# Performance work log

Hardware: AMD Instinct MI355X
Metric: run time of the kernel (lower is better)

## Reference

```python
import jax, jax.numpy as jnp
import numpy as np

B, T, I, H, L, O = 256, 512, 5, 100, 5, 3
BN_EPS = 1e-5


def _lstm_layer(xs, W_ih, W_hh, bias):
    """xs: [B,T,in] -> hidden seq [B,T,H]. PyTorch gate order i,f,g,o."""
    Bv = xs.shape[0]
    Hd = W_hh.shape[1]
    h0 = jnp.zeros((Bv, Hd), xs.dtype)
    c0 = jnp.zeros((Bv, Hd), xs.dtype)

    def step(carry, x_t):
        h, c = carry
        gates = x_t @ W_ih.T + h @ W_hh.T + bias  # [B,4H]
        i, f, g, o = jnp.split(gates, 4, axis=-1)
        i = jax.nn.sigmoid(i)
        f = jax.nn.sigmoid(f)
        g = jnp.tanh(g)
        o = jax.nn.sigmoid(o)
        c = f * c + i * g
        h = o * jnp.tanh(c)
        return (h, c), h

    _, hs = jax.lax.scan(step, (h0, c0), xs.transpose(1, 0, 2))  # hs: [T,B,H]
    return hs.transpose(1, 0, 2)


def setup_inputs() -> dict:
    key = jax.random.key(0)
    ks = jax.random.split(key, 12)
    s = 0.1  # weight scale to keep gates in a reasonable range
    return {
        "x": jax.random.normal(ks[0], (B, T, I), jnp.float32),
        "W_ih0": jax.random.normal(ks[1], (4 * H, I), jnp.float32) * s,
        "W_hh0": jax.random.normal(ks[2], (4 * H, H), jnp.float32) * s,
        "b0": jax.random.normal(ks[3], (4 * H,), jnp.float32) * s,
        "W_ih": jax.random.normal(ks[4], (L - 1, 4 * H, H), jnp.float32) * s,
        "W_hh": jax.random.normal(ks[5], (L - 1, 4 * H, H), jnp.float32) * s,
        "b": jax.random.normal(ks[6], (L - 1, 4 * H), jnp.float32) * s,
        "gamma": jnp.ones((H,), jnp.float32),
        "beta": jnp.zeros((H,), jnp.float32),
        "run_mean": jnp.zeros((H,), jnp.float32),
        "run_var": jnp.ones((H,), jnp.float32),
        "W1": jax.random.normal(ks[7], (H, H), jnp.float32) * s,
        "b1": jnp.zeros((H,), jnp.float32),
        "W2": jax.random.normal(ks[8], (H, H), jnp.float32) * s,
        "b2": jnp.zeros((H,), jnp.float32),
        "W3": jax.random.normal(ks[9], (O, H), jnp.float32) * s,
        "b3": jnp.zeros((O,), jnp.float32),
    }


def reference(x, W_ih0, W_hh0, b0, W_ih, W_hh, b,
              gamma, beta, run_mean, run_var,
              W1, b1, W2, b2, W3, b3):
    # 5-layer stacked LSTM (batch_first)
    h = _lstm_layer(x, W_ih0, W_hh0, b0)
    for l in range(L - 1):
        h = _lstm_layer(h, W_ih[l], W_hh[l], b[l])
    # dropout (eval mode -> identity), take last timestep
    last = h[:, -1, :]  # [B,H]
    # BatchNorm1d, eval mode (running statistics)
    xn = (last - run_mean) * jax.lax.rsqrt(run_var + BN_EPS) * gamma + beta
    # 3-layer MLP head with ReLU
    y = jax.nn.relu(xn @ W1.T + b1)
    y = jax.nn.relu(y @ W2.T + b2)
    return y @ W3.T + b3  # [B,O]
```

## Files before the change

kernel.cpp:

```cpp
#include <hip/hip_runtime.h>

#define NT 1024
#define TSEQ 512

typedef float float2v __attribute__((ext_vector_type(2)));

__device__ __forceinline__ float sigmoid_(float x) { return 1.0f / (1.0f + __expf(-x)); }
__device__ __forceinline__ float tanh_(float x) { return 1.0f - 2.0f / (1.0f + __expf(2.0f * x)); }

extern "C" __global__ void prep_weights(const float* __restrict__ Wih0,
                                        const float* __restrict__ Whh0,
                                        const float* __restrict__ WihL,
                                        const float* __restrict__ WhhL,
                                        float4* __restrict__ wbuf) {
    int gid = blockIdx.x * 256 + threadIdx.x;
    if (gid >= 102400) return;
    int tid = gid & 1023;
    int lgq = gid >> 10;
    int gq = lgq % 20;
    int l = lgq / 20;
    int g = gq / 5, q = gq % 5;
    float tmp[4] = {0.f, 0.f, 0.f, 0.f};
    if (tid < 1000) {
        int f = tid / 100, rg = tid % 100;
        int row = g * 100 + rg;
        int k0 = 20 * f + 4 * q;
        for (int c = 0; c < 4; ++c) {
            int k = k0 + c;
            float w = 0.f;
            if (l == 0) {
                if (k < 5) w = Wih0[row * 5 + k];
                else if (k < 105) w = Whh0[row * 100 + (k - 5)];
            } else {
                if (k < 100) w = WihL[(l - 1) * 40000 + row * 100 + k];
                else w = WhhL[(l - 1) * 40000 + row * 100 + (k - 100)];
            }
            tmp[c] = w;
        }
    }
    wbuf[gid] = make_float4(tmp[0], tmp[1], tmp[2], tmp[3]);
}

template <int IN, bool FIRST, bool STORE>
__device__ void run_layer(const float4* __restrict__ wl, const float* __restrict__ bL,
                          const float* __restrict__ xsrc, float* __restrict__ hdst,
                          int b, int tid, int f, int rg, bool real,
                          float* xh, float4* part4) {
    float2v w[40];
#pragma unroll
    for (int g = 0; g < 4; ++g) {
#pragma unroll
        for (int q = 0; q < 5; ++q) {
            float4 t = wl[(g * 5 + q) * 1024 + tid];
            w[g * 10 + 2 * q]     = (float2v){t.x, t.y};
            w[g * 10 + 2 * q + 1] = (float2v){t.z, t.w};
        }
    }
    float bi = 0.f, bf = 0.f, bg = 0.f, bo = 0.f;
    if (tid < 100) {
        bi = bL[tid]; bf = bL[100 + tid]; bg = bL[200 + tid]; bo = bL[300 + tid];
    }

    if (tid < 256) xh[tid] = 0.f;
    __syncthreads();
    if (FIRST) {
        if (tid < 5) xh[tid] = xsrc[b * TSEQ * 5 + tid];
    } else {
        if (tid < 25) ((float4*)xh)[tid] = ((const float4*)xsrc)[b * TSEQ * 25 + tid];
    }
    __syncthreads();

    const float4* xv4 = (const float4*)xh + f * 5;
    float c = 0.f, hprev = 0.f;

    for (int t = 0; t < TSEQ; ++t) {
        if (STORE) {
            if (tid < 100 && t > 0) hdst[(b * TSEQ + (t - 1)) * 100 + tid] = hprev;
        }
        int tn = (t + 1 < TSEQ) ? (t + 1) : (TSEQ - 1);
        float pfs = 0.f;
        float4 pf4 = {0.f, 0.f, 0.f, 0.f};
        if (FIRST) {
            if (tid >= 128 && tid < 133) pfs = xsrc[(b * TSEQ + tn) * 5 + (tid - 128)];
        } else {
            if (tid >= 128 && tid < 153) pf4 = ((const float4*)xsrc)[(b * TSEQ + tn) * 25 + (tid - 128)];
        }

        float2v a0 = {0.f, 0.f}, a1 = {0.f, 0.f}, a2 = {0.f, 0.f}, a3 = {0.f, 0.f};
#pragma unroll
        for (int q = 0; q < 5; ++q) {
            float4 xq = xv4[q];
            float2v xlo = (float2v){xq.x, xq.y};
            float2v xhi = (float2v){xq.z, xq.w};
            a0 = __builtin_elementwise_fma(w[2 * q],      xlo, a0);
            a0 = __builtin_elementwise_fma(w[2 * q + 1],  xhi, a0);
            a1 = __builtin_elementwise_fma(w[10 + 2 * q],     xlo, a1);
            a1 = __builtin_elementwise_fma(w[10 + 2 * q + 1], xhi, a1);
            a2 = __builtin_elementwise_fma(w[20 + 2 * q],     xlo, a2);
            a2 = __builtin_elementwise_fma(w[20 + 2 * q + 1], xhi, a2);
            a3 = __builtin_elementwise_fma(w[30 + 2 * q],     xlo, a3);
            a3 = __builtin_elementwise_fma(w[30 + 2 * q + 1], xhi, a3);
        }
        if (real) {
            part4[f * 100 + rg] = make_float4(a0.x + a0.y, a1.x + a1.y,
                                              a2.x + a2.y, a3.x + a3.y);
        }
        __syncthreads();

        if (tid < 100) {
            float4 s = part4[tid];
#pragma unroll
            for (int ff = 1; ff < 10; ++ff) {
                float4 tt = part4[ff * 100 + tid];
                s.x += tt.x; s.y += tt.y; s.z += tt.z; s.w += tt.w;
            }
            float gi = sigmoid_(s.x + bi);
            float gf = sigmoid_(s.y + bf);
            float gg = tanh_(s.z + bg);
            float go = sigmoid_(s.w + bo);
            c = gf * c + gi * gg;
            float hv = go * tanh_(c);
            xh[IN + tid] = hv;
            hprev = hv;
        }
        if (FIRST) {
            if (tid >= 128 && tid < 133) xh[tid - 128] = pfs;
        } else {
            if (tid >= 128 && tid < 153) ((float4*)xh)[tid - 128] = pf4;
        }
        __syncthreads();
    }
    if (STORE) {
        if (tid < 100) hdst[(b * TSEQ + TSEQ - 1) * 100 + tid] = hprev;
    }
}

extern "C" __global__ void __launch_bounds__(NT, 4)
gesture_lstm_kernel(const float* __restrict__ x,
                    const float4* __restrict__ wbuf,
                    const float* __restrict__ b0, const float* __restrict__ bLv,
                    const float* __restrict__ gamma, const float* __restrict__ beta,
                    const float* __restrict__ rmean, const float* __restrict__ rvar,
                    const float* __restrict__ W1, const float* __restrict__ b1,
                    const float* __restrict__ W2, const float* __restrict__ b2,
                    const float* __restrict__ W3, const float* __restrict__ b3,
                    float* __restrict__ out, float* __restrict__ hseq) {
    __shared__ __align__(16) float xh[256];
    __shared__ __align__(16) float4 part4[1000];
    __shared__ __align__(16) float hw[10000];

    int tid = threadIdx.x;
    int b = blockIdx.x;
    int f = tid / 100;
    int rg = tid % 100;
    bool real = tid < 1000;

    run_layer<5,   true,  true >(wbuf + 0 * 20480, b0,         x,    hseq, b, tid, f, rg, real, xh, part4);
    run_layer<100, false, true >(wbuf + 1 * 20480, bLv + 0,    hseq, hseq, b, tid, f, rg, real, xh, part4);
    run_layer<100, false, true >(wbuf + 2 * 20480, bLv + 400,  hseq, hseq, b, tid, f, rg, real, xh, part4);
    run_layer<100, false, true >(wbuf + 3 * 20480, bLv + 800,  hseq, hseq, b, tid, f, rg, real, xh, part4);
    run_layer<100, false, false>(wbuf + 4 * 20480, bLv + 1200, hseq, hseq, b, tid, f, rg, real, xh, part4);

    float* fcbuf = (float*)part4;
    if (tid < 100) {
        float hv = xh[100 + tid];
        xh[tid] = (hv - rmean[tid]) * rsqrtf(rvar[tid] + 1e-5f) * gamma[tid] + beta[tid];
    }
    __syncthreads();

    for (int i = tid; i < 2500; i += NT) ((float4*)hw)[i] = ((const float4*)W1)[i];
    __syncthreads();
    if (tid < 100) {
        float acc = b1[tid];
#pragma unroll
        for (int k = 0; k < 100; ++k) acc = fmaf(hw[tid * 100 + k], xh[k], acc);
        fcbuf[tid] = fmaxf(acc, 0.0f);
    }
    __syncthreads();

    for (int i = tid; i < 2500; i += NT) ((float4*)hw)[i] = ((const float4*)W2)[i];
    __syncthreads();
    if (tid < 100) {
        float acc = b2[tid];
#pragma unroll
        for (int k = 0; k < 100; ++k) acc = fmaf(hw[tid * 100 + k], fcbuf[k], acc);
        fcbuf[400 + tid] = fmaxf(acc, 0.0f);
    }
    __syncthreads();

    if (tid < 3) {
        float acc = b3[tid];
#pragma unroll
        for (int k = 0; k < 100; ++k) acc = fmaf(W3[tid * 100 + k], fcbuf[400 + k], acc);
        out[b * 3 + tid] = acc;
    }
}

extern "C" void kernel_launch(void* const* d_in, const int* in_sizes, int n_in,
                              void* d_out, int out_size, void* d_ws, size_t ws_size,
                              hipStream_t stream) {
    const float* x     = (const float*)d_in[0];
    const float* Wih0  = (const float*)d_in[1];
    const float* Whh0  = (const float*)d_in[2];
    const float* b0    = (const float*)d_in[3];
    const float* WihL  = (const float*)d_in[4];
    const float* WhhL  = (const float*)d_in[5];
    const float* bLv   = (const float*)d_in[6];
    const float* gamma = (const float*)d_in[7];
    const float* beta  = (const float*)d_in[8];
    const float* rmean = (const float*)d_in[9];
    const float* rvar  = (const float*)d_in[10];
    const float* W1    = (const float*)d_in[11];
    const float* b1    = (const float*)d_in[12];
    const float* W2    = (const float*)d_in[13];
    const float* b2    = (const float*)d_in[14];
    const float* W3    = (const float*)d_in[15];
    const float* b3    = (const float*)d_in[16];

    float4* wbuf = (float4*)d_ws;
    float* hseq  = (float*)((char*)d_ws + 102400 * 16);

    prep_weights<<<dim3(400), dim3(256), 0, stream>>>(Wih0, Whh0, WihL, WhhL, wbuf);
    gesture_lstm_kernel<<<dim3(256), dim3(NT), 0, stream>>>(
        x, wbuf, b0, bLv, gamma, beta, rmean, rvar, W1, b1, W2, b2, W3, b3,
        (float*)d_out, hseq);
}
```

Measured before the change: 2.435 ms.

## Replace LDS partial-sum reduction with DPP cross-lane reduction and double-buffered state

Reorganizes the per-step LSTM work so each group of 16 lanes owns two hidden units across all four gates, with the k-dimension split across the 16 lanes. Partial dot products are combined with DPP lane shuffles instead of being written to shared memory and summed by 100 threads. The hidden/input vector is double-buffered, which cuts the two barriers per timestep down to one. The block shrinks to 832 threads and each thread keeps 28 float4 weight registers, raising register pressure. The activation math is now done redundantly by all lanes.

Measured after the change: 9.624 ms. 3.95x slower.

```diff
diff --git a/kernel.cpp b/kernel.cpp
--- a/kernel.cpp
+++ b/kernel.cpp
@@ -1,12 +1,18 @@
 #include <hip/hip_runtime.h>
 
-#define NT 1024
+#define NT 832
 #define TSEQ 512
 
 typedef float float2v __attribute__((ext_vector_type(2)));
 
 __device__ __forceinline__ float sigmoid_(float x) { return 1.0f / (1.0f + __expf(-x)); }
 __device__ __forceinline__ float tanh_(float x) { return 1.0f - 2.0f / (1.0f + __expf(2.0f * x)); }
+
+template <int CTRL>
+__device__ __forceinline__ float dppmv(float x) {
+    return __int_as_float(__builtin_amdgcn_update_dpp(
+        0, __float_as_int(x), CTRL, 0xF, 0xF, true));
+}
 
 extern "C" __global__ void prep_weights(const float* __restrict__ Wih0,
                                         const float* __restrict__ Whh0,
@@ -14,28 +20,30 @@
                                         const float* __restrict__ WhhL,
                                         float4* __restrict__ wbuf) {
     int gid = blockIdx.x * 256 + threadIdx.x;
-    if (gid >= 102400) return;
-    int tid = gid & 1023;
-    int lgq = gid >> 10;
-    int gq = lgq % 20;
-    int l = lgq / 20;
-    int g = gq / 5, q = gq % 5;
+    if (gid >= 116480) return;
+    int tid = gid % 832;
+    int ql = gid / 832;
+    int q = ql % 28;
+    int l = ql / 28;
+    int p = tid / 16, f = tid % 16;
     float tmp[4] = {0.f, 0.f, 0.f, 0.f};
-    if (tid < 1000) {
-        int f = tid / 100, rg = tid % 100;
-        int row = g * 100 + rg;
-        int k0 = 20 * f + 4 * q;
-        for (int c = 0; c < 4; ++c) {
-            int k = k0 + c;
+    if (tid < 800) {
+        for (int j = 0; j < 4; ++j) {
+            int e = 4 * q + j;
+            int r = e / 14, cc = e % 14;
+            int unit = 2 * p + (r >= 4 ? 1 : 0);
+            int gate = r & 3;
+            int row = gate * 100 + unit;
+            int k = 14 * f + cc;
             float w = 0.f;
             if (l == 0) {
                 if (k < 5) w = Wih0[row * 5 + k];
                 else if (k < 105) w = Whh0[row * 100 + (k - 5)];
             } else {
                 if (k < 100) w = WihL[(l - 1) * 40000 + row * 100 + k];
-                else w = WhhL[(l - 1) * 40000 + row * 100 + (k - 100)];
+                else if (k < 200) w = WhhL[(l - 1) * 40000 + row * 100 + (k - 100)];
             }
-            tmp[c] = w;
+            tmp[j] = w;
         }
     }
     wbuf[gid] = make_float4(tmp[0], tmp[1], tmp[2], tmp[3]);
@@ -44,98 +52,102 @@
 template <int IN, bool FIRST, bool STORE>
 __device__ void run_layer(const float4* __restrict__ wl, const float* __restrict__ bL,
                           const float* __restrict__ xsrc, float* __restrict__ hdst,
-                          int b, int tid, int f, int rg, bool real,
-                          float* xh, float4* part4) {
-    float2v w[40];
-#pragma unroll
-    for (int g = 0; g < 4; ++g) {
-#pragma unroll
-        for (int q = 0; q < 5; ++q) {
-            float4 t = wl[(g * 5 + q) * 1024 + tid];
-            w[g * 10 + 2 * q]     = (float2v){t.x, t.y};
-            w[g * 10 + 2 * q + 1] = (float2v){t.z, t.w};
-        }
-    }
-    float bi = 0.f, bf = 0.f, bg = 0.f, bo = 0.f;
-    if (tid < 100) {
-        bi = bL[tid]; bf = bL[100 + tid]; bg = bL[200 + tid]; bo = bL[300 + tid];
-    }
-
-    if (tid < 256) xh[tid] = 0.f;
+                          int b, int tid, int f, int myu, bool real,
+                          float* bufs) {
+    float4 wq[28];
+#pragma unroll
+    for (int q = 0; q < 28; ++q) wq[q] = wl[q * 832 + tid];
+
+    float bi = 0.f, bff = 0.f, bgg = 0.f, boo = 0.f;
+    if (real) {
+        bi = bL[myu]; bff = bL[100 + myu]; bgg = bL[200 + myu]; boo = bL[300 + myu];
+    }
+
+    for (int i = tid; i < 448; i += NT) bufs[i] = 0.f;
     __syncthreads();
     if (FIRST) {
-        if (tid < 5) xh[tid] = xsrc[b * TSEQ * 5 + tid];
+        if (tid < 5) bufs[tid] = xsrc[b * TSEQ * 5 + tid];
     } else {
-        if (tid < 25) ((float4*)xh)[tid] = ((const float4*)xsrc)[b * TSEQ * 25 + tid];
-    }
-    __syncthreads();
-
-    const float4* xv4 = (const float4*)xh + f * 5;
+        if (tid < 25) ((float4*)bufs)[tid] = ((const float4*)xsrc)[b * TSEQ * 25 + tid];
+    }
+    __syncthreads();
+
     float c = 0.f, hprev = 0.f;
-
+#pragma unroll 1
     for (int t = 0; t < TSEQ; ++t) {
+        float* cur = bufs + (t & 1) * 224;
+        float* nxt = bufs + ((t + 1) & 1) * 224;
+
         if (STORE) {
-            if (tid < 100 && t > 0) hdst[(b * TSEQ + (t - 1)) * 100 + tid] = hprev;
-        }
-        int tn = (t + 1 < TSEQ) ? (t + 1) : (TSEQ - 1);
+            if (real && f < 2 && t > 0) hdst[(b * TSEQ + t - 1) * 100 + myu] = hprev;
+        }
+        int tn = (t + 1 < TSEQ) ? t + 1 : TSEQ - 1;
         float pfs = 0.f;
-        float4 pf4 = {0.f, 0.f, 0.f, 0.f};
+        float4 pf4 = make_float4(0.f, 0.f, 0.f, 0.f);
         if (FIRST) {
             if (tid >= 128 && tid < 133) pfs = xsrc[(b * TSEQ + tn) * 5 + (tid - 128)];
         } else {
             if (tid >= 128 && tid < 153) pf4 = ((const float4*)xsrc)[(b * TSEQ + tn) * 25 + (tid - 128)];
         }
 
-        float2v a0 = {0.f, 0.f}, a1 = {0.f, 0.f}, a2 = {0.f, 0.f}, a3 = {0.f, 0.f};
-#pragma unroll
-        for (int q = 0; q < 5; ++q) {
-            float4 xq = xv4[q];
-            float2v xlo = (float2v){xq.x, xq.y};
-            float2v xhi = (float2v){xq.z, xq.w};
-            a0 = __builtin_elementwise_fma(w[2 * q],      xlo, a0);
-            a0 = __builtin_elementwise_fma(w[2 * q + 1],  xhi, a0);
-            a1 = __builtin_elementwise_fma(w[10 + 2 * q],     xlo, a1);
-            a1 = __builtin_elementwise_fma(w[10 + 2 * q + 1], xhi, a1);
-            a2 = __builtin_elementwise_fma(w[20 + 2 * q],     xlo, a2);
-            a2 = __builtin_elementwise_fma(w[20 + 2 * q + 1], xhi, a2);
-            a3 = __builtin_elementwise_fma(w[30 + 2 * q],     xlo, a3);
-            a3 = __builtin_elementwise_fma(w[30 + 2 * q + 1], xhi, a3);
-        }
-        if (real) {
-            part4[f * 100 + rg] = make_float4(a0.x + a0.y, a1.x + a1.y,
-                                              a2.x + a2.y, a3.x + a3.y);
-        }
+        const float2v* xp = (const float2v*)(cur + 14 * f);
+        float2v xr[7];
+#pragma unroll
+        for (int i = 0; i < 7; ++i) xr[i] = xp[i];
+
+        float2v acc[8];
+#pragma unroll
+        for (int r = 0; r < 8; ++r) acc[r] = (float2v){0.f, 0.f};
+#pragma unroll
+        for (int cc = 0; cc < 7; ++cc) {
+#pragma unroll
+            for (int r = 0; r < 8; ++r) {
+                int e = r * 14 + 2 * cc;
+                float2v wp = ((e & 2) == 0) ? (float2v){wq[e >> 2].x, wq[e >> 2].y}
+                                            : (float2v){wq[e >> 2].z, wq[e >> 2].w};
+                acc[r] = __builtin_elementwise_fma(wp, xr[cc], acc[r]);
+            }
+        }
+        float a[8];
+#pragma unroll
+        for (int r = 0; r < 8; ++r) a[r] = acc[r].x + acc[r].y;
+
+#pragma unroll
+        for (int r = 0; r < 8; ++r) a[r] += dppmv<0xB1>(a[r]);
+#pragma unroll
+        for (int r = 0; r < 8; ++r) a[r] += dppmv<0x4E>(a[r]);
+#pragma unroll
+        for (int r = 0; r < 8; ++r) a[r] += dppmv<0x141>(a[r]);
+#pragma unroll
+        for (int r = 0; r < 8; ++r) a[r] += dppmv<0x140>(a[r]);
+
+        bool odd = (f & 1) != 0;
+        float si = (odd ? a[4] : a[0]) + bi;
+        float sf = (odd ? a[5] : a[1]) + bff;
+        float sg = (odd ? a[6] : a[2]) + bgg;
+        float so = (odd ? a[7] : a[3]) + boo;
+        float gi = sigmoid_(si);
+        float gf = sigmoid_(sf);
+        float gg = tanh_(sg);
+        float go = sigmoid_(so);
+        c = gf * c + gi * gg;
+        float hv = go * tanh_(c);
+
+        if (real && f < 2) nxt[IN + myu] = hv;
+        if (FIRST) {
+            if (tid >= 128 && tid < 133) nxt[tid - 128] = pfs;
+        } else {
+            if (tid >= 128 && tid < 153) ((float4*)nxt)[tid - 128] = pf4;
+        }
+        hprev = hv;
         __syncthreads();
-
-        if (tid < 100) {
-            float4 s = part4[tid];
-#pragma unroll
-            for (int ff = 1; ff < 10; ++ff) {
-                float4 tt = part4[ff * 100 + tid];
-                s.x += tt.x; s.y += tt.y; s.z += tt.z; s.w += tt.w;
-            }
-            float gi = sigmoid_(s.x + bi);
-            float gf = sigmoid_(s.y + bf);
-            float gg = tanh_(s.z + bg);
-            float go = sigmoid_(s.w + bo);
-            c = gf * c + gi * gg;
-            float hv = go * tanh_(c);
-            xh[IN + tid] = hv;
-            hprev = hv;
-        }
-        if (FIRST) {
-            if (tid >= 128 && tid < 133) xh[tid - 128] = pfs;
-        } else {
-            if (tid >= 128 && tid < 153) ((float4*)xh)[tid - 128] = pf4;
-        }
-        __syncthreads();
     }
     if (STORE) {
-        if (tid < 100) hdst[(b * TSEQ + TSEQ - 1) * 100 + tid] = hprev;
-    }
-}
-
-extern "C" __global__ void __launch_bounds__(NT, 4)
+        if (real && f < 2) hdst[(b * TSEQ + TSEQ - 1) * 100 + myu] = hprev;
+    }
+}
+
+extern "C" __global__ void __launch_bounds__(NT, 1)
 gesture_lstm_kernel(const float* __restrict__ x,
                     const float4* __restrict__ wbuf,
                     const float* __restrict__ b0, const float* __restrict__ bLv,
@@ -145,26 +157,25 @@
                     const float* __restrict__ W2, const float* __restrict__ b2,
                     const float* __restrict__ W3, const float* __restrict__ b3,
                     float* __restrict__ out, float* __restrict__ hseq) {
-    __shared__ __align__(16) float xh[256];
-    __shared__ __align__(16) float4 part4[1000];
+    __shared__ __align__(16) float bufs[448];
     __shared__ __align__(16) float hw[10000];
 
     int tid = threadIdx.x;
     int b = blockIdx.x;
-    int f = tid / 100;
-    int rg = tid % 100;
-    bool real = tid < 1000;
-
-    run_layer<5,   true,  true >(wbuf + 0 * 20480, b0,         x,    hseq, b, tid, f, rg, real, xh, part4);
-    run_layer<100, false, true >(wbuf + 1 * 20480, bLv + 0,    hseq, hseq, b, tid, f, rg, real, xh, part4);
-    run_layer<100, false, true >(wbuf + 2 * 20480, bLv + 400,  hseq, hseq, b, tid, f, rg, real, xh, part4);
-    run_layer<100, false, true >(wbuf + 3 * 20480, bLv + 800,  hseq, hseq, b, tid, f, rg, real, xh, part4);
-    run_layer<100, false, false>(wbuf + 4 * 20480, bLv + 1200, hseq, hseq, b, tid, f, rg, real, xh, part4);
-
-    float* fcbuf = (float*)part4;
+    int p = tid / 16;
+    int f = tid % 16;
+    int myu = 2 * p + (f & 1);
+    bool real = tid < 800;
+
+    run_layer<5,   true,  true >(wbuf + 0 * 23296, b0,         x,    hseq, b, tid, f, myu, real, bufs);
+    run_layer<100, false, true >(wbuf + 1 * 23296, bLv + 0,    hseq, hseq, b, tid, f, myu, real, bufs);
+    run_layer<100, false, true >(wbuf + 2 * 23296, bLv + 400,  hseq, hseq, b, tid, f, myu, real, bufs);
+    run_layer<100, false, true >(wbuf + 3 * 23296, bLv + 800,  hseq, hseq, b, tid, f, myu, real, bufs);
+    run_layer<100, false, false>(wbuf + 4 * 23296, bLv + 1200, hseq, hseq, b, tid, f, myu, real, bufs);
+
     if (tid < 100) {
-        float hv = xh[100 + tid];
-        xh[tid] = (hv - rmean[tid]) * rsqrtf(rvar[tid] + 1e-5f) * gamma[tid] + beta[tid];
+        float hv = bufs[100 + tid];
+        bufs[224 + tid] = (hv - rmean[tid]) * rsqrtf(rvar[tid] + 1e-5f) * gamma[tid] + beta[tid];
     }
     __syncthreads();
 
@@ -173,8 +184,8 @@
     if (tid < 100) {
         float acc = b1[tid];
 #pragma unroll
-        for (int k = 0; k < 100; ++k) acc = fmaf(hw[tid * 100 + k], xh[k], acc);
-        fcbuf[tid] = fmaxf(acc, 0.0f);
+        for (int k = 0; k < 100; ++k) acc = fmaf(hw[tid * 100 + k], bufs[224 + k], acc);
+        bufs[tid] = fmaxf(acc, 0.0f);
     }
     __syncthreads();
 
@@ -183,15 +194,15 @@
     if (tid < 100) {
         float acc = b2[tid];
 #pragma unroll
-        for (int k = 0; k < 100; ++k) acc = fmaf(hw[tid * 100 + k], fcbuf[k], acc);
-        fcbuf[400 + tid] = fmaxf(acc, 0.0f);
+        for (int k = 0; k < 100; ++k) acc = fmaf(hw[tid * 100 + k], bufs[k], acc);
+        bufs[224 + tid] = fmaxf(acc, 0.0f);
     }
     __syncthreads();
 
     if (tid < 3) {
         float acc = b3[tid];
 #pragma unroll
-        for (int k = 0; k < 100; ++k) acc = fmaf(W3[tid * 100 + k], fcbuf[400 + k], acc);
+        for (int k = 0; k < 100; ++k) acc = fmaf(W3[tid * 100 + k], bufs[224 + k], acc);
         out[b * 3 + tid] = acc;
     }
 }
@@ -218,9 +229,9 @@
     const float* b3    = (const float*)d_in[16];
 
     float4* wbuf = (float4*)d_ws;
-    float* hseq  = (float*)((char*)d_ws + 102400 * 16);
-
-    prep_weights<<<dim3(400), dim3(256), 0, stream>>>(Wih0, Whh0, WihL, WhhL, wbuf);
+    float* hseq  = (float*)((char*)d_ws + 116480 * 16);
+
+    prep_weights<<<dim3(455), dim3(256), 0, stream>>>(Wih0, Whh0, WihL, WhhL, wbuf);
     gesture_lstm_kernel<<<dim3(256), dim3(NT), 0, stream>>>(
         x, wbuf, b0, bLv, gamma, beta, rmean, rvar, W1, b1, W2, b2, W3, b3,
         (float*)d_out, hseq);
```
